# Kernel tuning notes

Hardware: AMD Instinct MI355X
Metric: run time of the kernel (lower is better)

## Reference

```python
import jax, jax.numpy as jnp
import numpy as np

# ---- module hyperparameters (from init_kwargs) ----
BOX = 256          # box_size
SIG = 1.5          # gaussian kernel sigma (pixels)
K = 9              # kernel_size = ceil(6*sig), made odd
HALF = K // 2
N = 50000          # n_points
LAT = 10           # latent_dim
NEUR = 32          # n_neurons
NLAYERS = 3        # n_layers
B = 16             # batch


def _uniform(key, shape, fan_in):
    a = 1.0 / np.sqrt(fan_in)
    return jax.random.uniform(key, shape, jnp.float32, -a, a)


def setup_inputs() -> dict:
    key = jax.random.key(0)
    ks = jax.random.split(key, 12)
    z = jax.random.normal(ks[0], (B, LAT), jnp.float32)
    # random proper rotation matrices via QR (faithful to cryo-EM poses)
    m = jax.random.normal(ks[1], (B, 3, 3), jnp.float32)
    q, _ = jnp.linalg.qr(m)
    r = q * jnp.sign(jnp.linalg.det(q))[:, None, None]
    ini = jnp.array([0.5, 0.5, 1.0], jnp.float32)
    pos_param = 0.1 * (jax.random.uniform(ks[2], (N, 3), jnp.float32) - ini)
    amp = 0.1 * jnp.ones((1,), jnp.float32)
    lin0_w = _uniform(ks[3], (NEUR, 3 + LAT - 1), 3 + LAT - 1)   # bias=False
    deform_w = _uniform(ks[4], (NLAYERS, NEUR, NEUR), NEUR)
    deform_b = _uniform(ks[5], (NLAYERS, NEUR), NEUR)
    lin1a_w = _uniform(ks[6], (3, NEUR), NEUR)                    # bias=False
    lin1b_w = _uniform(ks[7], (3, 3), 3)                          # bias=False
    linamp_w = _uniform(ks[8], (N, 1), 1)
    linamp_b = _uniform(ks[9], (N,), 1)
    return {"z": z, "r": r, "pos_param": pos_param, "amp": amp,
            "lin0_w": lin0_w, "deform_w": deform_w, "deform_b": deform_b,
            "lin1a_w": lin1a_w, "lin1b_w": lin1b_w,
            "linamp_w": linamp_w, "linamp_b": linamp_b, "d": 1}


def _splat(proj, amps):
    """Gaussian splat of points onto a BOXxBOX grid.
    proj: (B, N, 2) in [-0.5, 0.5];  amps: (B, N).  Returns (B, BOX, BOX)."""
    px = (proj + 0.5) * (BOX - 1)                  # pixel coords (B,N,2)
    c = jnp.floor(px + 0.5)                        # nearest pixel center
    off = jnp.arange(K, dtype=px.dtype) - HALF     # (K,)
    g0 = c[..., 0:1] + off                         # (B,N,K) grid coords dim0
    g1 = c[..., 1:2] + off                         # (B,N,K) grid coords dim1
    inv2s2 = 1.0 / (2.0 * SIG * SIG)
    w0 = jnp.exp(-(g0 - px[..., 0:1]) ** 2 * inv2s2)
    w1 = jnp.exp(-(g1 - px[..., 1:2]) ** 2 * inv2s2)
    w0 = w0 * ((g0 >= 0) & (g0 <= BOX - 1))       # mask out-of-bounds taps
    w1 = w1 * ((g1 >= 0) & (g1 <= BOX - 1))
    vals = amps[..., None, None] * w0[..., :, None] * w1[..., None, :]  # (B,N,K,K)
    i0 = jnp.clip(g0, 0, BOX - 1).astype(jnp.int32)
    i1 = jnp.clip(g1, 0, BOX - 1).astype(jnp.int32)

    def scat(i0b, i1b, vb):                        # per image scatter-add
        iy = jnp.broadcast_to(i0b[:, :, None], vb.shape).reshape(-1)
        ix = jnp.broadcast_to(i1b[:, None, :], vb.shape).reshape(-1)
        return jnp.zeros((BOX, BOX), vb.dtype).at[iy, ix].add(vb.reshape(-1))

    return jax.vmap(scat)(i0, i1, vals)


def _forward(z, r, pos_param, amp, lin0_w, deform_w, deform_b,
             lin1a_w, lin1b_w, linamp_w, linamp_b, d):
    bsz = z.shape[0]
    posi = jnp.broadcast_to(pos_param, (bsz, N, 3))
    if d > 0:
        conf = jnp.broadcast_to(z[:, None, :-1], (bsz, N, LAT - 1))
        h = jnp.concatenate([posi, conf], axis=-1) @ lin0_w.T   # (B,N,NEUR)
        for l in range(NLAYERS):                                # residual relu blocks
            h = jax.nn.relu(h @ deform_w[l].T + deform_b[l]) + h
        res = jnp.tanh(h @ lin1a_w.T) @ lin1b_w.T               # (B,N,3)
        pos = posi + res
    else:
        res = jnp.zeros_like(posi)
        pos = posi
    amp_corr = jax.nn.sigmoid(z[:, -1:] @ linamp_w.T + linamp_b)  # (B,N)
    proj_pos = jnp.einsum('bnj,bjk->bnk', pos, r)[..., :2]        # rotate + project
    amps = amp_corr * amp[0]
    img = _splat(proj_pos, amps)
    return img, img, proj_pos, pos, res


def reference(z, r, pos_param, amp, lin0_w, deform_w, deform_b,
              lin1a_w, lin1b_w, linamp_w, linamp_b, d):
    return _forward(z, r, pos_param, amp, lin0_w, deform_w, deform_b,
                    lin1a_w, lin1b_w, linamp_w, linamp_b, d)
```

## Files before the change

kernel.cpp:

```cpp
#include <hip/hip_runtime.h>
#include <math.h>

#define BOX   256
#define NPTS  50000
#define LATD  10
#define NEUR  32
#define NLAY  3
#define BATCH 16

#define MTPB  256
#define MBLKX ((NPTS + MTPB - 1)/MTPB)

#define PTPB  256
#define PBLKX ((NPTS + PTPB - 1)/PTPB)

#define CELLS_X 64
#define CELLS   (CELLS_X*CELLS_X)
#define PREF_STRIDE 4104
#define CHUNK   128
#define WCAP    4608

#define GBLK    256
#define GSTRIDE (GBLK*4)

#define IMG_ELEMS (BATCH*BOX*BOX)
#define OFF_IMG2  (IMG_ELEMS)
#define OFF_PROJ  (2*IMG_ELEMS)
#define OFF_POS   (OFF_PROJ + BATCH*NPTS*2)
#define OFF_RES   (OFF_POS  + BATCH*NPTS*3)

#define WS_COUNTS 0
#define WS_NWORK  (BATCH*CELLS)
#define WS_PREFIX (WS_NWORK + BATCH)
#define WS_WORK   (WS_PREFIX + BATCH*PREF_STRIDE)
#define WS_AUX    (WS_WORK + BATCH*WCAP)
#define WS_INTS   (WS_AUX + BATCH*NPTS)

#define HSTR 36

typedef _Float16 f16x8 __attribute__((ext_vector_type(8)));
typedef float    f32x4 __attribute__((ext_vector_type(4)));

#if __has_builtin(__builtin_amdgcn_exp2f)
#define EXP2R(x) __builtin_amdgcn_exp2f(x)
#else
#define EXP2R(x) exp2f(x)
#endif

__device__ __forceinline__ float fast_tanh(float x) {
    return 1.0f - 2.0f / (__expf(2.0f * x) + 1.0f);
}

__device__ __forceinline__ f16x8 pack8h(f32x4 a, f32x4 b) {
    f16x8 v;
    v[0] = (_Float16)a[0]; v[1] = (_Float16)a[1];
    v[2] = (_Float16)a[2]; v[3] = (_Float16)a[3];
    v[4] = (_Float16)b[0]; v[5] = (_Float16)b[1];
    v[6] = (_Float16)b[2]; v[7] = (_Float16)b[3];
    return v;
}

__global__ __launch_bounds__(MTPB) void mlp_bin(
    const float* __restrict__ z, const float* __restrict__ r,
    const float* __restrict__ pos_param, const float* __restrict__ amp,
    const float* __restrict__ lin0_w, const float* __restrict__ deform_w,
    const float* __restrict__ deform_b, const float* __restrict__ lin1a_w,
    const float* __restrict__ lin1b_w, const float* __restrict__ linamp_w,
    const float* __restrict__ linamp_b, const int* __restrict__ dflag,
    float* __restrict__ out, int* __restrict__ counts, int* __restrict__ aux)
{
    __shared__ __align__(16) float s_mem[4*64*HSTR + NEUR];
    int*   s_cnt = (int*)s_mem;
    float* s_z   = s_mem + 4*64*HSTR;

    const int b     = blockIdx.y;
    const int tid   = threadIdx.x;
    const int wave  = tid >> 6;
    const int lane  = tid & 63;
    const int cfrag = lane & 15;
    const int rq    = lane >> 4;
    const int k0    = rq * 8;
    float* __restrict__ s_hw = s_mem + wave*64*HSTR;

    if (tid < NEUR) {
        float acc = 0.f;
        #pragma unroll
        for (int j = 0; j < LATD-1; j++)
            acc = fmaf(lin0_w[tid*12 + 3 + j], z[b*LATD + j], acc);
        s_z[tid] = acc;
    }
    __syncthreads();

    const int n  = blockIdx.x*MTPB + tid;
    const bool v0 = (n < NPTS);
    const int m0 = v0 ? n : (NPTS-1);
    const int dd = *dflag;

    const float p0w = pos_param[m0*3+0], p1w = pos_param[m0*3+1], p2w = pos_param[m0*3+2];

    float res0 = 0.f, res1 = 0.f, res2 = 0.f;

    if (dd > 0) {
        f16x8 bfrag[NLAY][2];
        float bias_c[NLAY][2];
        #pragma unroll
        for (int l = 0; l < NLAY; ++l) {
            #pragma unroll
            for (int nt = 0; nt < 2; ++nt) {
                const int c = cfrag + 16*nt;
                const float* wp = deform_w + l*NEUR*NEUR + c*NEUR + k0;
                bfrag[l][nt]  = pack8h(*(const f32x4*)wp, *(const f32x4*)(wp + 4));
                bias_c[l][nt] = deform_b[l*NEUR + c];
            }
        }

        #pragma unroll
        for (int o4 = 0; o4 < 8; ++o4) {
            f32x4 hv;
            #pragma unroll
            for (int jj = 0; jj < 4; ++jj) {
                const int o = o4*4 + jj;
                hv[jj] = fmaf(lin0_w[o*12+0], p0w,
                         fmaf(lin0_w[o*12+1], p1w,
                         fmaf(lin0_w[o*12+2], p2w, s_z[o])));
            }
            *(f32x4*)&s_hw[lane*HSTR + o4*4] = hv;
        }
        __syncthreads();

        float rs0[4][4], rs1[4][4];
        #pragma unroll
        for (int mt = 0; mt < 4; ++mt) {
            const int rb = (16*mt + 4*rq)*HSTR + cfrag;
            #pragma unroll
            for (int rr = 0; rr < 4; ++rr) {
                rs0[mt][rr] = s_hw[rb + rr*HSTR];
                rs1[mt][rr] = s_hw[rb + rr*HSTR + 16];
            }
        }

        const f32x4 zc = {0.f, 0.f, 0.f, 0.f};
        #pragma unroll
        for (int l = 0; l < NLAY; ++l) {
            f16x8 af[4];
            #pragma unroll
            for (int mt = 0; mt < 4; ++mt) {
                const float* ap = &s_hw[(16*mt + cfrag)*HSTR + k0];
                af[mt] = pack8h(*(const f32x4*)ap, *(const f32x4*)(ap + 4));
            }
            f32x4 ac0[4], ac1[4];
            #pragma unroll
            for (int mt = 0; mt < 4; ++mt) {
                ac0[mt] = __builtin_amdgcn_mfma_f32_16x16x32_f16(af[mt], bfrag[l][0], zc, 0, 0, 0);
                ac1[mt] = __builtin_amdgcn_mfma_f32_16x16x32_f16(af[mt], bfrag[l][1], zc, 0, 0, 0);
            }
            __syncthreads();
            const float b0l = bias_c[l][0], b1l = bias_c[l][1];
            #pragma unroll
            for (int mt = 0; mt < 4; ++mt) {
                const int rb = (16*mt + 4*rq)*HSTR + cfrag;
                #pragma unroll
                for (int rr = 0; rr < 4; ++rr) {
                    const float h0n = fmaxf(ac0[mt][rr] + b0l, 0.f) + rs0[mt][rr];
                    const float h1n = fmaxf(ac1[mt][rr] + b1l, 0.f) + rs1[mt][rr];
                    rs0[mt][rr] = h0n;
                    rs1[mt][rr] = h1n;
                    s_hw[rb + rr*HSTR]      = h0n;
                    s_hw[rb + rr*HSTR + 16] = h1n;
                }
            }
            __syncthreads();
        }

        float t0 = 0.f, t1 = 0.f, t2 = 0.f;
        #pragma unroll
        for (int ch = 0; ch < 8; ++ch) {
            const f32x4 hv = *(const f32x4*)&s_hw[lane*HSTR + ch*4];
            #pragma unroll
            for (int jj = 0; jj < 4; ++jj) {
                const int j = ch*4 + jj;
                t0 = fmaf(lin1a_w[0*NEUR + j], hv[jj], t0);
                t1 = fmaf(lin1a_w[1*NEUR + j], hv[jj], t1);
                t2 = fmaf(lin1a_w[2*NEUR + j], hv[jj], t2);
            }
        }
        t0 = fast_tanh(t0); t1 = fast_tanh(t1); t2 = fast_tanh(t2);
        res0 = fmaf(t0, lin1b_w[0], fmaf(t1, lin1b_w[1], t2*lin1b_w[2]));
        res1 = fmaf(t0, lin1b_w[3], fmaf(t1, lin1b_w[4], t2*lin1b_w[5]));
        res2 = fmaf(t0, lin1b_w[6], fmaf(t1, lin1b_w[7], t2*lin1b_w[8]));
    }

    const float r00 = r[b*9+0], r01 = r[b*9+1];
    const float r10 = r[b*9+3], r11 = r[b*9+4];
    const float r20 = r[b*9+6], r21 = r[b*9+7];

    int cell = 0;
    if (v0) {
        const float pos0 = p0w + res0, pos1 = p1w + res1, pos2 = p2w + res2;
        const float pj0 = fmaf(pos0, r00, fmaf(pos1, r10, pos2*r20));
        const float pj1 = fmaf(pos0, r01, fmaf(pos1, r11, pos2*r21));
        const long long bn = (long long)b*NPTS + n;
        out[OFF_PROJ + bn*2 + 0] = pj0;  out[OFF_PROJ + bn*2 + 1] = pj1;
        out[OFF_POS  + bn*3 + 0] = pos0; out[OFF_POS  + bn*3 + 1] = pos1;
        out[OFF_POS  + bn*3 + 2] = pos2;
        out[OFF_RES  + bn*3 + 0] = res0; out[OFF_RES + bn*3 + 1] = res1;
        out[OFF_RES  + bn*3 + 2] = res2;
        const float px0 = (pj0 + 0.5f) * (float)(BOX-1);
        const float px1 = (pj1 + 0.5f) * (float)(BOX-1);
        const int c0 = (int)fminf(fmaxf(floorf(px0 + 0.5f), 0.f), 255.f);
        const int c1 = (int)fminf(fmaxf(floorf(px1 + 0.5f), 0.f), 255.f);
        cell = (c0>>2)*CELLS_X + (c1>>2);
    }

    __syncthreads();
    for (int i = tid; i < CELLS; i += MTPB) s_cnt[i] = 0;
    __syncthreads();
    int rank = 0;
    if (v0) rank = atomicAdd(&s_cnt[cell], 1);
    __syncthreads();
    for (int c = tid; c < CELLS; c += MTPB) {
        const int cnt = s_cnt[c];
        if (cnt > 0) s_cnt[c] = atomicAdd(&counts[b*CELLS + c], cnt);
    }
    __syncthreads();
    if (v0) aux[b*NPTS + n] = (cell << 16) | (s_cnt[cell] + rank);
}

__global__ __launch_bounds__(1024) void scan_cells(
    const int* __restrict__ counts, int* __restrict__ prefix,
    int* __restrict__ n_work, int* __restrict__ work)
{
    __shared__ int lds[1024];
    __shared__ int s_nw;
    const int img = blockIdx.x, t = threadIdx.x;
    if (t == 0) s_nw = 0;
    const int4 v = ((const int4*)(counts + img*CELLS))[t];
    const int s0 = v.x, s1 = s0 + v.y, s2 = s1 + v.z, s3 = s2 + v.w;
    lds[t] = s3;
    __syncthreads();
    #pragma unroll 1
    for (int off = 1; off < 1024; off <<= 1) {
        const int add = (t >= off) ? lds[t - off] : 0;
        __syncthreads();
        lds[t] += add;
        __syncthreads();
    }
    const int incl = lds[t];
    const int base = incl - s3;
    ((int4*)(prefix + img*PREF_STRIDE))[t] = make_int4(base, base+s0, base+s1, base+s2);
    if (t == 1023) prefix[img*PREF_STRIDE + CELLS] = incl;

    const int cnts[4] = { v.x, v.y, v.z, v.w };
    #pragma unroll
    for (int i = 0; i < 4; i++) {
        const int cnt = cnts[i];
        if (cnt > 0) {
            const int c = 4*t + i;
            const int nch = (cnt + CHUNK - 1)/CHUNK;
            const int wb = atomicAdd(&s_nw, nch);
            for (int k = 0; k < nch; k++) work[img*WCAP + wb + k] = (c << 9) | k;
        }
    }
    __syncthreads();
    if (t == 0) n_work[img] = s_nw;
}

__global__ __launch_bounds__(PTPB) void place(
    const float* __restrict__ z, const float* __restrict__ amp,
    const float* __restrict__ linamp_w, const float* __restrict__ linamp_b,
    const float* __restrict__ out, const int* __restrict__ prefix,
    const int* __restrict__ aux, float4* __restrict__ recs)
{
    const int b = blockIdx.y;
    const int n = blockIdx.x*PTPB + threadIdx.x;
    if (n >= NPTS) return;

    const long long bn = (long long)b*NPTS + n;
    const float pj0 = out[OFF_PROJ + bn*2 + 0];
    const float pj1 = out[OFF_PROJ + bn*2 + 1];
    const float lo = fmaf(z[b*LATD + LATD-1], linamp_w[n], linamp_b[n]);
    const float a  = amp[0] / (1.0f + __expf(-lo));
    const float px0 = (pj0 + 0.5f) * (float)(BOX-1);
    const float px1 = (pj1 + 0.5f) * (float)(BOX-1);

    const int av  = aux[b*NPTS + n];
    const int cell = av >> 16, wr = av & 0xFFFF;
    const int dst  = prefix[b*PREF_STRIDE + cell] + wr;
    recs[(long long)b*NPTS + dst] = make_float4(px0, px1, a, 0.f);
}

__global__ __launch_bounds__(256) void gather_work(
    const float4* __restrict__ recs, const int* __restrict__ prefix,
    const int* __restrict__ n_work, const int* __restrict__ work,
    float* __restrict__ out)
{
    const int b    = blockIdx.y;
    const int wave = blockIdx.x*4 + (threadIdx.x >> 6);
    const int lane = threadIdx.x & 63;
    const int nw   = n_work[b];

    const int* __restrict__ P = prefix + b*PREF_STRIDE;
    const float4* __restrict__ R = recs + (long long)b*NPTS;
    float* __restrict__ img = out + (size_t)b*BOX*BOX;
    const float Kc  = -0.32059884f;
    const float K8  = 8.0f  * Kc;
    const float K16 = 16.0f * Kc;
    const float C32 = 0.00081582472f;

    for (int it = wave; it < nw; it += GSTRIDE) {
        const int wd   = __builtin_amdgcn_readfirstlane(work[b*WCAP + it]);
        const int cell = wd >> 9, kch = wd & 511;
        const int s = P[cell] + kch*CHUNK;
        const int e = min(P[cell+1], s + CHUNK);

        const int cy = cell >> 6, cx = cell & 63;
        const int col = lane & 15, r0 = lane >> 4;
        const int gx  = 4*cx - 4 + col;
        const int gy0 = 4*cy - 4 + r0;
        const float xf  = (float)gx;
        const float y0f = (float)gy0;
        const float frc = (float)(r0 + 4*cy);

        float a0 = 0.f, a1 = 0.f, a2 = 0.f;
        #pragma unroll 8
        for (int rr = s; rr < e; ++rr) {
            const float4 rc = R[rr];
            const float ry = rc.x, rx = rc.y, ra = rc.z;

            const float dx = xf - rx;
            const float dy = y0f - ry;
            const float d2 = fmaf(dy, dy, dx*dx);
            float g = ra * EXP2R(d2 * Kc);
            g = (dx > -4.5f && dx <= 4.5f) ? g : 0.f;

            const float u  = EXP2R(fminf(fmaf(dy, K8, K16), 126.f));
            const float stf = floorf(ry + 0.5f);
            const float uu  = (u * u) * C32;
            const float g0m = (frc >= stf) ? g  : 0.f;
            const float u2m = (frc <= stf) ? uu : 0.f;
            a0 += g0m;
            a1 = fmaf(g, u,   a1);
            a2 = fmaf(g, u2m, a2);
        }

        if (gx >= 0 && gx < BOX) {
            if (a0 != 0.f && gy0 >= 0)      atomicAdd(&img[ gy0     *BOX + gx], a0);
            if (a1 != 0.f)                  atomicAdd(&img[(gy0 + 4)*BOX + gx], a1);
            if (a2 != 0.f && gy0 + 8 < BOX) atomicAdd(&img[(gy0 + 8)*BOX + gx], a2);
        }
    }
}

__global__ __launch_bounds__(256) void copy_img(const float4* __restrict__ src,
                                                float4* __restrict__ dst, int n4)
{
    int i = blockIdx.x*blockDim.x + threadIdx.x;
    if (i < n4) dst[i] = src[i];
}

extern "C" void kernel_launch(void* const* d_in, const int* in_sizes, int n_in,
                              void* d_out, int out_size, void* d_ws, size_t ws_size,
                              hipStream_t stream)
{
    const float* z        = (const float*)d_in[0];
    const float* r        = (const float*)d_in[1];
    const float* posp     = (const float*)d_in[2];
    const float* amp      = (const float*)d_in[3];
    const float* lin0_w   = (const float*)d_in[4];
    const float* deform_w = (const float*)d_in[5];
    const float* deform_b = (const float*)d_in[6];
    const float* lin1a_w  = (const float*)d_in[7];
    const float* lin1b_w  = (const float*)d_in[8];
    const float* linamp_w = (const float*)d_in[9];
    const float* linamp_b = (const float*)d_in[10];
    const int*   dflag    = (const int*)d_in[11];
    float* out = (float*)d_out;

    int* ws_i    = (int*)d_ws;
    int* counts  = ws_i + WS_COUNTS;
    int* n_work  = ws_i + WS_NWORK;
    int* prefix  = ws_i + WS_PREFIX;
    int* work    = ws_i + WS_WORK;
    int* aux     = ws_i + WS_AUX;
    float4* recs = (float4*)((char*)d_ws + (size_t)WS_INTS*sizeof(int));

    hipMemsetAsync(counts, 0, (size_t)(BATCH*CELLS + BATCH)*sizeof(int), stream);
    hipMemsetAsync(out, 0, (size_t)IMG_ELEMS*sizeof(float), stream);

    dim3 gridM(MBLKX, BATCH);
    mlp_bin<<<gridM, MTPB, 0, stream>>>(z, r, posp, amp, lin0_w, deform_w, deform_b,
                                        lin1a_w, lin1b_w, linamp_w, linamp_b, dflag,
                                        out, counts, aux);

    scan_cells<<<BATCH, 1024, 0, stream>>>(counts, prefix, n_work, work);

    dim3 gridP(PBLKX, BATCH);
    place<<<gridP, PTPB, 0, stream>>>(z, amp, linamp_w, linamp_b, out, prefix, aux, recs);

    dim3 gridG(GBLK, BATCH);
    gather_work<<<gridG, 256, 0, stream>>>(recs, prefix, n_work, work, out);

    const int n4 = IMG_ELEMS/4;
    copy_img<<<(n4 + 255)/256, 256, 0, stream>>>((const float4*)out,
                                                 (float4*)(out + OFF_IMG2), n4);
}
```

Measured before the change: 190.6 us.

## Use fp16 LDS activations, shuffle-based scan, and atomic work-stealing in gather

The MLP hidden state is now kept in LDS as fp16 rather than fp32, so MFMA A-fragments load directly without repacking and LDS footprint shrinks. The cell-count scan is rewritten from a 1024-step LDS Hillis-Steele loop into wave shuffles plus a small cross-wave scan. The gather kernel switches from a static grid-stride loop to dynamic work-stealing through an atomic cursor, which reuses the counts buffer and is reset inside place; its grid is halved. The per-point rounded row is precomputed in place and stored in the record's spare slot, and the exp clamp and range test are simplified. Risks include extra fp16 rounding of residual activations and contention on the atomic cursor.

```diff
diff --git a/kernel.cpp b/kernel.cpp
--- a/kernel.cpp
+++ b/kernel.cpp
@@ -20,8 +20,7 @@
 #define CHUNK   128
 #define WCAP    4608
 
-#define GBLK    256
-#define GSTRIDE (GBLK*4)
+#define GBLK    128
 
 #define IMG_ELEMS (BATCH*BOX*BOX)
 #define OFF_IMG2  (IMG_ELEMS)
@@ -36,9 +35,10 @@
 #define WS_AUX    (WS_WORK + BATCH*WCAP)
 #define WS_INTS   (WS_AUX + BATCH*NPTS)
 
-#define HSTR 36
+#define HSTRH 40
 
 typedef _Float16 f16x8 __attribute__((ext_vector_type(8)));
+typedef _Float16 f16x4 __attribute__((ext_vector_type(4)));
 typedef float    f32x4 __attribute__((ext_vector_type(4)));
 
 #if __has_builtin(__builtin_amdgcn_exp2f)
@@ -49,15 +49,6 @@
 
 __device__ __forceinline__ float fast_tanh(float x) {
     return 1.0f - 2.0f / (__expf(2.0f * x) + 1.0f);
-}
-
-__device__ __forceinline__ f16x8 pack8h(f32x4 a, f32x4 b) {
-    f16x8 v;
-    v[0] = (_Float16)a[0]; v[1] = (_Float16)a[1];
-    v[2] = (_Float16)a[2]; v[3] = (_Float16)a[3];
-    v[4] = (_Float16)b[0]; v[5] = (_Float16)b[1];
-    v[6] = (_Float16)b[2]; v[7] = (_Float16)b[3];
-    return v;
 }
 
 __global__ __launch_bounds__(MTPB) void mlp_bin(
@@ -69,9 +60,10 @@
     const float* __restrict__ linamp_b, const int* __restrict__ dflag,
     float* __restrict__ out, int* __restrict__ counts, int* __restrict__ aux)
 {
-    __shared__ __align__(16) float s_mem[4*64*HSTR + NEUR];
-    int*   s_cnt = (int*)s_mem;
-    float* s_z   = s_mem + 4*64*HSTR;
+    __shared__ __align__(16) unsigned char s_raw[4*64*HSTRH*2 + NEUR*4];
+    _Float16* s_h   = (_Float16*)s_raw;
+    float*    s_z   = (float*)(s_raw + 4*64*HSTRH*2);
+    int*      s_cnt = (int*)s_raw;
 
     const int b     = blockIdx.y;
     const int tid   = threadIdx.x;
@@ -80,7 +72,7 @@
     const int cfrag = lane & 15;
     const int rq    = lane >> 4;
     const int k0    = rq * 8;
-    float* __restrict__ s_hw = s_mem + wave*64*HSTR;
+    _Float16* __restrict__ s_hw = s_h + wave*64*HSTRH;
 
     if (tid < NEUR) {
         float acc = 0.f;
@@ -109,33 +101,40 @@
             for (int nt = 0; nt < 2; ++nt) {
                 const int c = cfrag + 16*nt;
                 const float* wp = deform_w + l*NEUR*NEUR + c*NEUR + k0;
-                bfrag[l][nt]  = pack8h(*(const f32x4*)wp, *(const f32x4*)(wp + 4));
+                const f32x4 w0 = *(const f32x4*)wp;
+                const f32x4 w1 = *(const f32x4*)(wp + 4);
+                f16x8 bv;
+                bv[0]=(_Float16)w0[0]; bv[1]=(_Float16)w0[1];
+                bv[2]=(_Float16)w0[2]; bv[3]=(_Float16)w0[3];
+                bv[4]=(_Float16)w1[0]; bv[5]=(_Float16)w1[1];
+                bv[6]=(_Float16)w1[2]; bv[7]=(_Float16)w1[3];
+                bfrag[l][nt]  = bv;
                 bias_c[l][nt] = deform_b[l*NEUR + c];
             }
         }
 
         #pragma unroll
         for (int o4 = 0; o4 < 8; ++o4) {
-            f32x4 hv;
+            f16x4 h4;
             #pragma unroll
             for (int jj = 0; jj < 4; ++jj) {
                 const int o = o4*4 + jj;
-                hv[jj] = fmaf(lin0_w[o*12+0], p0w,
-                         fmaf(lin0_w[o*12+1], p1w,
-                         fmaf(lin0_w[o*12+2], p2w, s_z[o])));
-            }
-            *(f32x4*)&s_hw[lane*HSTR + o4*4] = hv;
+                h4[jj] = (_Float16)fmaf(lin0_w[o*12+0], p0w,
+                                   fmaf(lin0_w[o*12+1], p1w,
+                                   fmaf(lin0_w[o*12+2], p2w, s_z[o])));
+            }
+            *(f16x4*)&s_hw[lane*HSTRH + o4*4] = h4;
         }
         __syncthreads();
 
         float rs0[4][4], rs1[4][4];
         #pragma unroll
         for (int mt = 0; mt < 4; ++mt) {
-            const int rb = (16*mt + 4*rq)*HSTR + cfrag;
             #pragma unroll
             for (int rr = 0; rr < 4; ++rr) {
-                rs0[mt][rr] = s_hw[rb + rr*HSTR];
-                rs1[mt][rr] = s_hw[rb + rr*HSTR + 16];
+                const int row = 16*mt + 4*rq + rr;
+                rs0[mt][rr] = (float)s_hw[row*HSTRH + cfrag];
+                rs1[mt][rr] = (float)s_hw[row*HSTRH + cfrag + 16];
             }
         }
 
@@ -144,10 +143,8 @@
         for (int l = 0; l < NLAY; ++l) {
             f16x8 af[4];
             #pragma unroll
-            for (int mt = 0; mt < 4; ++mt) {
-                const float* ap = &s_hw[(16*mt + cfrag)*HSTR + k0];
-                af[mt] = pack8h(*(const f32x4*)ap, *(const f32x4*)(ap + 4));
-            }
+            for (int mt = 0; mt < 4; ++mt)
+                af[mt] = *(const f16x8*)&s_hw[(16*mt + cfrag)*HSTRH + k0];
             f32x4 ac0[4], ac1[4];
             #pragma unroll
             for (int mt = 0; mt < 4; ++mt) {
@@ -158,15 +155,15 @@
             const float b0l = bias_c[l][0], b1l = bias_c[l][1];
             #pragma unroll
             for (int mt = 0; mt < 4; ++mt) {
-                const int rb = (16*mt + 4*rq)*HSTR + cfrag;
                 #pragma unroll
                 for (int rr = 0; rr < 4; ++rr) {
+                    const int row = 16*mt + 4*rq + rr;
                     const float h0n = fmaxf(ac0[mt][rr] + b0l, 0.f) + rs0[mt][rr];
                     const float h1n = fmaxf(ac1[mt][rr] + b1l, 0.f) + rs1[mt][rr];
                     rs0[mt][rr] = h0n;
                     rs1[mt][rr] = h1n;
-                    s_hw[rb + rr*HSTR]      = h0n;
-                    s_hw[rb + rr*HSTR + 16] = h1n;
+                    s_hw[row*HSTRH + cfrag]      = (_Float16)h0n;
+                    s_hw[row*HSTRH + cfrag + 16] = (_Float16)h1n;
                 }
             }
             __syncthreads();
@@ -174,14 +171,15 @@
 
         float t0 = 0.f, t1 = 0.f, t2 = 0.f;
         #pragma unroll
-        for (int ch = 0; ch < 8; ++ch) {
-            const f32x4 hv = *(const f32x4*)&s_hw[lane*HSTR + ch*4];
-            #pragma unroll
-            for (int jj = 0; jj < 4; ++jj) {
-                const int j = ch*4 + jj;
-                t0 = fmaf(lin1a_w[0*NEUR + j], hv[jj], t0);
-                t1 = fmaf(lin1a_w[1*NEUR + j], hv[jj], t1);
-                t2 = fmaf(lin1a_w[2*NEUR + j], hv[jj], t2);
+        for (int ch = 0; ch < 4; ++ch) {
+            const f16x8 hv = *(const f16x8*)&s_hw[lane*HSTRH + ch*8];
+            #pragma unroll
+            for (int jj = 0; jj < 8; ++jj) {
+                const int j = ch*8 + jj;
+                const float hf = (float)hv[jj];
+                t0 = fmaf(lin1a_w[0*NEUR + j], hf, t0);
+                t1 = fmaf(lin1a_w[1*NEUR + j], hf, t1);
+                t2 = fmaf(lin1a_w[2*NEUR + j], hf, t2);
             }
         }
         t0 = fast_tanh(t0); t1 = fast_tanh(t1); t2 = fast_tanh(t2);
@@ -230,24 +228,37 @@
     const int* __restrict__ counts, int* __restrict__ prefix,
     int* __restrict__ n_work, int* __restrict__ work)
 {
-    __shared__ int lds[1024];
+    __shared__ int wsum[16];
     __shared__ int s_nw;
     const int img = blockIdx.x, t = threadIdx.x;
+    const int lane = t & 63, wid = t >> 6;
     if (t == 0) s_nw = 0;
     const int4 v = ((const int4*)(counts + img*CELLS))[t];
-    const int s0 = v.x, s1 = s0 + v.y, s2 = s1 + v.z, s3 = s2 + v.w;
-    lds[t] = s3;
-    __syncthreads();
-    #pragma unroll 1
-    for (int off = 1; off < 1024; off <<= 1) {
-        const int add = (t >= off) ? lds[t - off] : 0;
-        __syncthreads();
-        lds[t] += add;
-        __syncthreads();
-    }
-    const int incl = lds[t];
+    const int s3 = v.x + v.y + v.z + v.w;
+
+    int sc = s3;
+    #pragma unroll
+    for (int off = 1; off < 64; off <<= 1) {
+        const int u = __shfl_up(sc, off, 64);
+        if (lane >= off) sc += u;
+    }
+    if (lane == 63) wsum[wid] = sc;
+    __syncthreads();
+    if (wid == 0) {
+        int ws = (lane < 16) ? wsum[lane] : 0;
+        #pragma unroll
+        for (int off = 1; off < 16; off <<= 1) {
+            const int u = __shfl_up(ws, off, 64);
+            if (lane >= off) ws += u;
+        }
+        if (lane < 16) wsum[lane] = ws;
+    }
+    __syncthreads();
+    const int woff = (wid > 0) ? wsum[wid-1] : 0;
+    const int incl = sc + woff;
     const int base = incl - s3;
-    ((int4*)(prefix + img*PREF_STRIDE))[t] = make_int4(base, base+s0, base+s1, base+s2);
+    ((int4*)(prefix + img*PREF_STRIDE))[t] =
+        make_int4(base, base+v.x, base+v.x+v.y, base+v.x+v.y+v.z);
     if (t == 1023) prefix[img*PREF_STRIDE + CELLS] = incl;
 
     const int cnts[4] = { v.x, v.y, v.z, v.w };
@@ -269,9 +280,10 @@
     const float* __restrict__ z, const float* __restrict__ amp,
     const float* __restrict__ linamp_w, const float* __restrict__ linamp_b,
     const float* __restrict__ out, const int* __restrict__ prefix,
-    const int* __restrict__ aux, float4* __restrict__ recs)
+    const int* __restrict__ aux, float4* __restrict__ recs, int* __restrict__ cursors)
 {
     const int b = blockIdx.y;
+    if (blockIdx.x == 0 && threadIdx.x == 0) cursors[b*64] = 0;
     const int n = blockIdx.x*PTPB + threadIdx.x;
     if (n >= NPTS) return;
 
@@ -286,18 +298,18 @@
     const int av  = aux[b*NPTS + n];
     const int cell = av >> 16, wr = av & 0xFFFF;
     const int dst  = prefix[b*PREF_STRIDE + cell] + wr;
-    recs[(long long)b*NPTS + dst] = make_float4(px0, px1, a, 0.f);
+    recs[(long long)b*NPTS + dst] = make_float4(px0, px1, a, floorf(px0 + 0.5f));
 }
 
 __global__ __launch_bounds__(256) void gather_work(
     const float4* __restrict__ recs, const int* __restrict__ prefix,
     const int* __restrict__ n_work, const int* __restrict__ work,
-    float* __restrict__ out)
+    float* __restrict__ out, int* __restrict__ cursors)
 {
     const int b    = blockIdx.y;
-    const int wave = blockIdx.x*4 + (threadIdx.x >> 6);
     const int lane = threadIdx.x & 63;
     const int nw   = n_work[b];
+    int* __restrict__ cur = cursors + b*64;
 
     const int* __restrict__ P = prefix + b*PREF_STRIDE;
     const float4* __restrict__ R = recs + (long long)b*NPTS;
@@ -307,7 +319,12 @@
     const float K16 = 16.0f * Kc;
     const float C32 = 0.00081582472f;
 
-    for (int it = wave; it < nw; it += GSTRIDE) {
+    for (;;) {
+        int grab;
+        if (lane == 0) grab = atomicAdd(cur, 1);
+        const int it = __shfl(grab, 0, 64);
+        if (it >= nw) break;
+
         const int wd   = __builtin_amdgcn_readfirstlane(work[b*WCAP + it]);
         const int cell = wd >> 9, kch = wd & 511;
         const int s = P[cell] + kch*CHUNK;
@@ -325,17 +342,16 @@
         #pragma unroll 8
         for (int rr = s; rr < e; ++rr) {
             const float4 rc = R[rr];
-            const float ry = rc.x, rx = rc.y, ra = rc.z;
+            const float ry = rc.x, rx = rc.y, ra = rc.z, stf = rc.w;
 
             const float dx = xf - rx;
             const float dy = y0f - ry;
             const float d2 = fmaf(dy, dy, dx*dx);
             float g = ra * EXP2R(d2 * Kc);
-            g = (dx > -4.5f && dx <= 4.5f) ? g : 0.f;
-
-            const float u  = EXP2R(fminf(fmaf(dy, K8, K16), 126.f));
-            const float stf = floorf(ry + 0.5f);
-            const float uu  = (u * u) * C32;
+            g = (fabsf(dx) <= 4.5f) ? g : 0.f;
+
+            const float u  = EXP2R(fminf(fmaf(dy, K8, K16), 60.f));
+            const float uu = (u * u) * C32;
             const float g0m = (frc >= stf) ? g  : 0.f;
             const float u2m = (frc <= stf) ? uu : 0.f;
             a0 += g0m;
@@ -395,10 +411,11 @@
     scan_cells<<<BATCH, 1024, 0, stream>>>(counts, prefix, n_work, work);
 
     dim3 gridP(PBLKX, BATCH);
-    place<<<gridP, PTPB, 0, stream>>>(z, amp, linamp_w, linamp_b, out, prefix, aux, recs);
+    place<<<gridP, PTPB, 0, stream>>>(z, amp, linamp_w, linamp_b, out, prefix, aux,
+                                      recs, counts);
 
     dim3 gridG(GBLK, BATCH);
-    gather_work<<<gridG, 256, 0, stream>>>(recs, prefix, n_work, work, out);
+    gather_work<<<gridG, 256, 0, stream>>>(recs, prefix, n_work, work, out, counts);
 
     const int n4 = IMG_ELEMS/4;
     copy_img<<<(n4 + 255)/256, 256, 0, stream>>>((const float4*)out,
```

Result: no change. 193.7 us (+1.6%).
